# Kernel tuning notes

Hardware: AMD Instinct MI355X
Metric: run time of the kernel (lower is better)

The kernel has to match this reference:

```python
import math
import jax, jax.numpy as jnp
import numpy as np

N_EMBD = 1024
N_HEAD = 16
HEAD_DIM = N_EMBD // N_HEAD


def setup_inputs() -> dict:
    key = jax.random.key(0)
    ks = jax.random.split(key, 5)
    B, S = 4, 2048
    x = jax.random.normal(ks[0], (B, S, 2, N_EMBD), dtype=jnp.float32)
    Wt = jax.random.normal(ks[1], (N_EMBD, 3 * N_EMBD), dtype=jnp.float32) * 0.02
    Ws = jax.random.normal(ks[2], (N_EMBD, 2 * N_EMBD), dtype=jnp.float32) * 0.02
    Wo = jax.random.normal(ks[3], (N_EMBD, N_EMBD), dtype=jnp.float32) * 0.02
    lam_ts = jnp.ones((1,), dtype=jnp.float32)
    lam_st = jnp.ones((1,), dtype=jnp.float32)
    lam_ss = jnp.ones((1,), dtype=jnp.float32)
    return {"x": x, "Wt": Wt, "Ws": Ws, "Wo": Wo,
            "lam_ts": lam_ts, "lam_st": lam_st, "lam_ss": lam_ss}


def _heads(t, B, S):
    # [B,S,E] -> [B,H,S,D]
    return t.reshape(B, S, N_HEAD, HEAD_DIM).transpose(0, 2, 1, 3)


def reference(x, Wt, Ws, Wo, lam_ts, lam_st, lam_ss):
    B, S, _, E = x.shape
    xt = x[:, :, 0, :]  # text stream [B,S,E]
    xs = x[:, :, 1, :]  # spatial stream [B,S,E]

    qt, kt, vt = jnp.split(xt @ Wt, 3, axis=-1)
    qs, ks = jnp.split(xs @ Ws, 2, axis=-1)
    qt, kt, vt = _heads(qt, B, S), _heads(kt, B, S), _heads(vt, B, S)
    qs, ks = _heads(qs, B, S), _heads(ks, B, S)

    scale = 1.0 / math.sqrt(HEAD_DIM)
    att = (jnp.einsum('bhqd,bhkd->bhqk', qt, kt)
           + lam_ts[0] * jnp.einsum('bhqd,bhkd->bhqk', qt, ks)
           + lam_st[0] * jnp.einsum('bhqd,bhkd->bhqk', qs, kt)
           + lam_ss[0] * jnp.einsum('bhqd,bhkd->bhqk', qs, ks)) * scale
    att = jax.nn.softmax(att, axis=-1)

    y = jnp.einsum('bhqk,bhkd->bhqd', att, vt)  # [B,H,S,D]
    y = y.transpose(0, 2, 1, 3).reshape(B, S, E)
    y = y @ Wo
    # concat text output with untouched spatial stream -> [B,S,2,E]
    return jnp.concatenate([y[:, :, None, :], xs[:, :, None, :]], axis=2)
```

## Files before the change

### kernel.cpp

```cpp
#include <hip/hip_runtime.h>

typedef short  short8  __attribute__((ext_vector_type(8)));
typedef float  f32x4   __attribute__((ext_vector_type(4)));
typedef ushort u16x4   __attribute__((ext_vector_type(4)));

__device__ __forceinline__ float bf2f(ushort u) {
  union { unsigned u; float f; } v; v.u = ((unsigned)u) << 16; return v.f;
}
__device__ __forceinline__ ushort f2bf(float f) {
  union { float f; unsigned u; } v; v.f = f;
  unsigned r = v.u + 0x7FFF + ((v.u >> 16) & 1);
  return (ushort)(r >> 16);
}
__device__ __forceinline__ float exp2_fast(float x) {
  float r; asm("v_exp_f32 %0, %1" : "=v"(r) : "v"(x)); return r;
}

__device__ __forceinline__ void gload16(const ushort* g, ushort* l) {
  __builtin_amdgcn_global_load_lds(
      (__attribute__((address_space(1))) void*)(void*)(const_cast<ushort*>(g)),
      (__attribute__((address_space(3))) void*)(void*)l, 16, 0, 0);
}


__global__ __launch_bounds__(256) void prep_x(const float* __restrict__ x,
                                              ushort* __restrict__ xt,
                                              ushort* __restrict__ xs,
                                              float* __restrict__ out) {
  size_t i = ((size_t)blockIdx.x * 256 + threadIdx.x) * 4;
  size_t m = i >> 10, e = i & 1023;
  f32x4 a = *(const f32x4*)&x[m * 2048 + e];
  f32x4 b = *(const f32x4*)&x[m * 2048 + 1024 + e];
  u16x4 ta, tb;
#pragma unroll
  for (int j = 0; j < 4; ++j) { ta[j] = f2bf(a[j]); tb[j] = f2bf(b[j]); }
  *(u16x4*)&xt[i] = ta;
  *(u16x4*)&xs[i] = tb;
  *(f32x4*)&out[m * 2048 + 1024 + e] = b;
}

__global__ __launch_bounds__(256) void transpose_w(const float* __restrict__ W,
                                                   ushort* __restrict__ Wt,
                                                   int K, int N, int nq,
                                                   float qscale) {
  __shared__ float tile[32][33];
  int n0 = blockIdx.x * 32, k0 = blockIdx.y * 32;
  int tx = threadIdx.x & 31, ty = threadIdx.x >> 5;
#pragma unroll
  for (int i = 0; i < 32; i += 8)
    tile[ty + i][tx] = W[(size_t)(k0 + ty + i) * N + n0 + tx];
  __syncthreads();
#pragma unroll
  for (int i = 0; i < 32; i += 8) {
    int n = n0 + ty + i;
    float v = tile[tx][ty + i];
    if (n < nq) v *= qscale;
    Wt[(size_t)n * K + k0 + tx] = f2bf(v);
  }
}

template <int EPI>
__global__ __launch_bounds__(256) void gemm_bt(const ushort* __restrict__ A,
                                               const ushort* __restrict__ Bt,
                                               int N,
                                               ushort* __restrict__ o1,
                                               ushort* __restrict__ o2,
                                               const ushort* __restrict__ ct2,
                                               float* __restrict__ of,
                                               const float* plts,
                                               const float* plst,
                                               const float* plss) {
  const int K = 1024;
  __shared__ ushort sA[128 * 32];
  __shared__ ushort sB[128 * 32];
  const int tid = threadIdx.x;
  const int wave = tid >> 6, lane = tid & 63;
  const int wr = wave >> 1, wc = wave & 1;
  const int l15 = lane & 15, l4 = lane >> 4;
  const int m0 = blockIdx.y * 128, n0 = blockIdx.x * 128;

  f32x4 acc[4][4];
  const f32x4 z = {0.f, 0.f, 0.f, 0.f};
#pragma unroll
  for (int a = 0; a < 4; ++a)
#pragma unroll
    for (int b = 0; b < 4; ++b) acc[a][b] = z;

  for (int k0 = 0; k0 < K; k0 += 32) {
#pragma unroll
    for (int j = 0; j < 2; ++j) {
      int cb = j * 256 + wave * 64;
      int c = cb + lane;
      int row = c >> 2, cc = c & 3;
      gload16(&A [(size_t)(m0 + row) * K + k0 + cc * 8], &sA[cb * 8]);
      gload16(&Bt[(size_t)(n0 + row) * K + k0 + cc * 8], &sB[cb * 8]);
    }
    __syncthreads();
    short8 af[4], bfr[4];
#pragma unroll
    for (int i = 0; i < 4; ++i) {
      af[i]  = *(const short8*)&sA[(wr * 64 + i * 16 + l15) * 32 + l4 * 8];
      bfr[i] = *(const short8*)&sB[(wc * 64 + i * 16 + l15) * 32 + l4 * 8];
    }
#pragma unroll
    for (int mi = 0; mi < 4; ++mi)
#pragma unroll
      for (int ni = 0; ni < 4; ++ni)
        acc[mi][ni] = __builtin_amdgcn_mfma_f32_16x16x32_bf16(af[mi], bfr[ni], acc[mi][ni], 0, 0, 0);
    __syncthreads();
  }

  float lts = 0.f, lst = 0.f, lss = 0.f;
  if constexpr (EPI == 2) { lts = plts[0]; lst = plst[0]; lss = plss[0]; }

#pragma unroll
  for (int mi = 0; mi < 4; ++mi)
#pragma unroll
    for (int ni = 0; ni < 4; ++ni) {
      int rowb = m0 + wr * 64 + mi * 16 + l4 * 4;
      int col  = n0 + wc * 64 + ni * 16 + l15;
      if constexpr (EPI == 0) {
#pragma unroll
        for (int r = 0; r < 4; ++r)
          of[(size_t)(rowb + r) * 2048 + col] = acc[mi][ni][r];
      } else if constexpr (EPI == 1) {
        if (col < 1024) {
          int h = col >> 6, d = col & 63;
#pragma unroll
          for (int r = 0; r < 4; ++r) {
            int s = rowb + r, b = s >> 11, ss = s & 2047;
            o1[((size_t)(b * 16 + h) * 2048 + ss) * 128 + d] = f2bf(acc[mi][ni][r]);
          }
        } else {
#pragma unroll
          for (int r = 0; r < 4; ++r)
            o2[(size_t)(rowb + r) * 2048 + (col - 1024)] = f2bf(acc[mi][ni][r]);
        }
      } else {
        if (col < 1024) {
          int h = col >> 6, d = col & 63;
#pragma unroll
          for (int r = 0; r < 4; ++r) {
            int s = rowb + r, b = s >> 11, ss = s & 2047;
            o1[((size_t)(b * 16 + h) * 2048 + ss) * 128 + 64 + d] = f2bf(acc[mi][ni][r]);
          }
        } else {
          int d64 = col - 1024, h = d64 >> 6, d = d64 & 63;
#pragma unroll
          for (int r = 0; r < 4; ++r) {
            int s = rowb + r, b = s >> 11, ss = s & 2047;
            float kt = bf2f(ct2[(size_t)s * 2048 + d64]);
            float ks = acc[mi][ni][r];
            float k1 = kt + lts * ks;
            float k2 = lst * kt + lss * ks;
            size_t base = ((size_t)(b * 16 + h) * 2048 + ss) * 128;
            int off = ((((d >> 3) ^ (ss & 7)) << 3)) + (d & 7);
            o2[base + off]      = f2bf(k1);
            o2[base + 64 + off] = f2bf(k2);
          }
        }
      }
    }
}

__global__ __launch_bounds__(256) void transpose_v(const ushort* __restrict__ Ct2,
                                                   ushort* __restrict__ Vt) {
  int bh = blockIdx.y; int s0 = blockIdx.x * 64;
  int b = bh >> 4, h = bh & 15;
  __shared__ ushort t[64][72];
  int tid = threadIdx.x;
#pragma unroll
  for (int j = 0; j < 2; ++j) {
    int c = j * 256 + tid;
    int srow = c >> 3, cc = c & 7;
    *(short8*)&t[srow][cc * 8] =
        *(const short8*)&Ct2[(size_t)(b * 2048 + s0 + srow) * 2048 + 1024 + h * 64 + cc * 8];
  }
  __syncthreads();
#pragma unroll
  for (int j = 0; j < 2; ++j) {
    int c = j * 256 + tid;
    int drow = c >> 3, cc = c & 7;
    short8 v;
#pragma unroll
    for (int k = 0; k < 8; ++k) v[k] = t[cc * 8 + k][drow];
    *(short8*)&Vt[((size_t)bh * 64 + drow) * 2048 + s0 + ((cc ^ (drow & 7)) * 8)] = v;
  }
}

__global__ __launch_bounds__(256) void attn_kernel(const ushort* __restrict__ Q,
                                                   const ushort* __restrict__ Kg,
                                                   const ushort* __restrict__ Vg,
                                                   ushort* __restrict__ Y) {
  const int id   = blockIdx.x;
  const int virt = (id & 7) * 128 + (id >> 3);
  const int bh = virt >> 4;
  const int q0 = (virt & 15) * 128;
  const int tid = threadIdx.x;
  const int wave = tid >> 6, lane = tid & 63;
  const int l15 = lane & 15, l4 = lane >> 4;
  const size_t qkb = (size_t)bh * 2048 * 128;
  const size_t vb  = (size_t)bh * 64 * 2048;

  __shared__ ushort sKV[2 * 64 * 128 + 64 * 64];
  ushort* const sK0 = sKV;
  ushort* const sV  = sKV + 2 * 64 * 128;

  auto stageK = [&](int kv0, int bufi) {
    ushort* dK = sK0 + bufi * (64 * 128);
#pragma unroll
    for (int j = 0; j < 4; ++j) {
      int base = j * 256 + wave * 64;
      int c = base + lane, row = c >> 4, cc = c & 15;
      gload16(&Kg[qkb + (size_t)(kv0 + row) * 128 + cc * 8], &dK[base * 8]);
    }
  };
  auto stageV = [&](int kv0) {
#pragma unroll
    for (int j = 0; j < 2; ++j) {
      int base = j * 256 + wave * 64;
      int c = base + lane, row = c >> 3, cc = c & 7;
      gload16(&Vg[vb + (size_t)row * 2048 + kv0 + cc * 8], &sV[base * 8]);
    }
  };

  short8 qf[2][4];
#pragma unroll
  for (int qi = 0; qi < 2; ++qi) {
    int qrow = q0 + wave * 32 + qi * 16 + l15;
#pragma unroll
    for (int kk = 0; kk < 4; ++kk)
      qf[qi][kk] = *(const short8*)&Q[qkb + (size_t)qrow * 128 + kk * 32 + l4 * 8];
  }
  const f32x4 z = {0.f, 0.f, 0.f, 0.f};
  f32x4 accO[2][4] = {{z, z, z, z}, {z, z, z, z}};
  float mrow[2] = {-3.0e38f, -3.0e38f}, lrow[2] = {0.f, 0.f};

  stageK(0, 0);
  stageV(0);
  __syncthreads();

  for (int t = 0; t < 32; ++t) {
    const int cur = t & 1;
    if (t < 31) stageK((t + 1) * 64, cur ^ 1);
    const ushort* cK = sK0 + cur * (64 * 128);

    f32x4 sc[2][4] = {{z, z, z, z}, {z, z, z, z}};
    __builtin_amdgcn_s_setprio(1);
#pragma unroll
    for (int kk = 0; kk < 4; ++kk)
#pragma unroll
      for (int kb = 0; kb < 4; ++kb) {
        int row = kb * 16 + l15;
        const short8 kf = *(const short8*)&cK[row * 128 + (((kk * 4 + l4) ^ (row & 7)) * 8)];
        sc[0][kb] = __builtin_amdgcn_mfma_f32_16x16x32_bf16(kf, qf[0][kk], sc[0][kb], 0, 0, 0);
        sc[1][kb] = __builtin_amdgcn_mfma_f32_16x16x32_bf16(kf, qf[1][kk], sc[1][kb], 0, 0, 0);
      }
    __builtin_amdgcn_s_setprio(0);

    union { uint u4[4]; short8 s8; } pa[2][2];
#pragma unroll
    for (int qi = 0; qi < 2; ++qi) {
      float mx = sc[qi][0][0];
#pragma unroll
      for (int kb = 0; kb < 4; ++kb)
#pragma unroll
        for (int r = 0; r < 4; ++r) mx = fmaxf(mx, sc[qi][kb][r]);
      mx = fmaxf(mx, __shfl_xor(mx, 16));
      mx = fmaxf(mx, __shfl_xor(mx, 32));

      if (__any(mx > mrow[qi] + 8.f)) {
        float mnew = fmaxf(mrow[qi], mx);
        float corr = exp2_fast(mrow[qi] - mnew);
        mrow[qi] = mnew;
        lrow[qi] *= corr;
#pragma unroll
        for (int r = 0; r < 4; ++r) {
          float cq = __shfl(corr, l4 * 4 + r);
#pragma unroll
          for (int nf = 0; nf < 4; ++nf) accO[qi][nf][r] *= cq;
        }
      }

      float ps = 0.f;
#pragma unroll
      for (int kb = 0; kb < 4; ++kb)
#pragma unroll
        for (int r = 0; r < 4; ++r) {
          float e = exp2_fast(sc[qi][kb][r] - mrow[qi]);
          sc[qi][kb][r] = e; ps += e;
        }
      lrow[qi] += ps;

      uint u00, u01, u10, u11, u20, u21, u30, u31;
#define CVTPK(d, a, b) asm("v_cvt_pk_bf16_f32 %0, %1, %2" : "=v"(d) : "v"(a), "v"(b))
      CVTPK(u00, sc[qi][0][0], sc[qi][0][1]); CVTPK(u01, sc[qi][0][2], sc[qi][0][3]);
      CVTPK(u10, sc[qi][1][0], sc[qi][1][1]); CVTPK(u11, sc[qi][1][2], sc[qi][1][3]);
      CVTPK(u20, sc[qi][2][0], sc[qi][2][1]); CVTPK(u21, sc[qi][2][2], sc[qi][2][3]);
      CVTPK(u30, sc[qi][3][0], sc[qi][3][1]); CVTPK(u31, sc[qi][3][2], sc[qi][3][3]);
#undef CVTPK
      asm volatile("v_permlane32_swap_b32 %0, %1" : "+v"(u00), "+v"(u10));
      asm volatile("v_permlane32_swap_b32 %0, %1" : "+v"(u01), "+v"(u11));
      asm volatile("v_permlane32_swap_b32 %0, %1" : "+v"(u20), "+v"(u30));
      asm volatile("v_permlane32_swap_b32 %0, %1" : "+v"(u21), "+v"(u31));
      asm volatile("v_permlane16_swap_b32 %0, %1" : "+v"(u00), "+v"(u10));
      asm volatile("v_permlane16_swap_b32 %0, %1" : "+v"(u01), "+v"(u11));
      asm volatile("v_permlane16_swap_b32 %0, %1" : "+v"(u20), "+v"(u30));
      asm volatile("v_permlane16_swap_b32 %0, %1" : "+v"(u21), "+v"(u31));
      pa[qi][0].u4[0] = u00; pa[qi][0].u4[1] = u01; pa[qi][0].u4[2] = u10; pa[qi][0].u4[3] = u11;
      pa[qi][1].u4[0] = u20; pa[qi][1].u4[1] = u21; pa[qi][1].u4[2] = u30; pa[qi][1].u4[3] = u31;
    }

    __syncthreads();

    __builtin_amdgcn_s_setprio(1);
#pragma unroll
    for (int nf = 0; nf < 4; ++nf) {
      int d = nf * 16 + l15;
      const short8 vf0 = *(const short8*)&sV[d * 64 + ((l4 ^ (d & 7)) * 8)];
      const short8 vf1 = *(const short8*)&sV[d * 64 + (((4 + l4) ^ (d & 7)) * 8)];
      accO[0][nf] = __builtin_amdgcn_mfma_f32_16x16x32_bf16(pa[0][0].s8, vf0, accO[0][nf], 0, 0, 0);
      accO[1][nf] = __builtin_amdgcn_mfma_f32_16x16x32_bf16(pa[1][0].s8, vf0, accO[1][nf], 0, 0, 0);
      accO[0][nf] = __builtin_amdgcn_mfma_f32_16x16x32_bf16(pa[0][1].s8, vf1, accO[0][nf], 0, 0, 0);
      accO[1][nf] = __builtin_amdgcn_mfma_f32_16x16x32_bf16(pa[1][1].s8, vf1, accO[1][nf], 0, 0, 0);
    }
    __builtin_amdgcn_s_setprio(0);

    __syncthreads();
    if (t < 31) stageV((t + 1) * 64);
  }

  int b = bh >> 4, hh = bh & 15;
#pragma unroll
  for (int qi = 0; qi < 2; ++qi) {
    float ls = lrow[qi] + __shfl_xor(lrow[qi], 16);
    ls += __shfl_xor(ls, 32);
    float linv = 1.f / ls;
#pragma unroll
    for (int r = 0; r < 4; ++r) {
      float lq = __shfl(linv, l4 * 4 + r);
      int q = q0 + wave * 32 + qi * 16 + l4 * 4 + r;
#pragma unroll
      for (int nf = 0; nf < 4; ++nf)
        Y[((size_t)b * 2048 + q) * 1024 + hh * 64 + nf * 16 + l15] =
            f2bf(accO[qi][nf][r] * lq);
    }
  }
}

extern "C" void kernel_launch(void* const* d_in, const int* in_sizes, int n_in,
                              void* d_out, int out_size, void* d_ws, size_t ws_size,
                              hipStream_t stream) {
  const float* x   = (const float*)d_in[0];
  const float* Wt  = (const float*)d_in[1];
  const float* Ws  = (const float*)d_in[2];
  const float* Wo  = (const float*)d_in[3];
  const float* lts = (const float*)d_in[4];
  const float* lst = (const float*)d_in[5];
  const float* lss = (const float*)d_in[6];
  float* out = (float*)d_out;
  char* ws = (char*)d_ws;

  ushort* xt    = (ushort*)(ws + 0);
  ushort* xs    = (ushort*)(ws + 16777216);
  ushort* Wt_bt = (ushort*)(ws + 33554432);
  ushort* Ws_bt = (ushort*)(ws + 39845888);
  ushort* Wo_bt = (ushort*)(ws + 44040192);
  ushort* Ct2   = (ushort*)(ws + 46137344);
  ushort* Qbuf  = (ushort*)(ws + 79691776);
  ushort* Kbuf  = (ushort*)(ws + 113246208);
  ushort* Vtbuf = (ushort*)(ws + 146800640);
  ushort* Ybuf  = (ushort*)(ws + 163577856);
  (void)in_sizes; (void)n_in; (void)out_size; (void)ws_size;

  const float qscale = 0.125f * 1.44269504f;

  prep_x<<<8192, 256, 0, stream>>>(x, xt, xs, out);
  transpose_w<<<dim3(96, 32), 256, 0, stream>>>(Wt, Wt_bt, 1024, 3072, 1024, qscale);
  transpose_w<<<dim3(64, 32), 256, 0, stream>>>(Ws, Ws_bt, 1024, 2048, 1024, qscale);
  transpose_w<<<dim3(32, 32), 256, 0, stream>>>(Wo, Wo_bt, 1024, 1024, 0, 1.f);
  gemm_bt<1><<<dim3(24, 64), 256, 0, stream>>>(xt, Wt_bt, 3072, Qbuf, Ct2,
                                               nullptr, nullptr, nullptr, nullptr, nullptr);
  gemm_bt<2><<<dim3(16, 64), 256, 0, stream>>>(xs, Ws_bt, 2048, Qbuf, Kbuf,
                                               Ct2, nullptr, lts, lst, lss);
  transpose_v<<<dim3(32, 64), 256, 0, stream>>>(Ct2, Vtbuf);
  attn_kernel<<<1024, 256, 0, stream>>>(Qbuf, Kbuf, Vtbuf, Ybuf);
  gemm_bt<0><<<dim3(8, 64), 256, 0, stream>>>(Ybuf, Wo_bt, 1024, nullptr, nullptr,
                                              nullptr, out, nullptr, nullptr, nullptr);
}
```

Measured before the change: 323.8 us.

## Replace QKV projection GEMMs with 256x256 double-buffered pipelined kernel

The two input-projection GEMMs now use a new 512-thread kernel with 256x256 output tiles and K-step 64. LDS is double-buffered and XOR-swizzled, global-to-LDS loads for the next K tile are interleaved between MFMA phases, and block IDs are remapped across XCDs. The aim is more data reuse per tile and overlap of memory latency with compute. In exchange it uses 128KB of LDS and many accumulator registers, and the grids are small (384 and 256 blocks), so occupancy and tail effects are a risk. The output projection keeps the old 128x128 kernel, split out as a non-templated version.

```diff
diff --git a/kernel.cpp b/kernel.cpp
--- a/kernel.cpp
+++ b/kernel.cpp
@@ -59,17 +59,9 @@
   }
 }
 
-template <int EPI>
-__global__ __launch_bounds__(256) void gemm_bt(const ushort* __restrict__ A,
-                                               const ushort* __restrict__ Bt,
-                                               int N,
-                                               ushort* __restrict__ o1,
-                                               ushort* __restrict__ o2,
-                                               const ushort* __restrict__ ct2,
-                                               float* __restrict__ of,
-                                               const float* plts,
-                                               const float* plst,
-                                               const float* plss) {
+__global__ __launch_bounds__(256) void gemm_bt0(const ushort* __restrict__ A,
+                                                const ushort* __restrict__ Bt,
+                                                float* __restrict__ of) {
   const int K = 1024;
   __shared__ ushort sA[128 * 32];
   __shared__ ushort sB[128 * 32];
@@ -110,31 +102,134 @@
     __syncthreads();
   }
 
+#pragma unroll
+  for (int mi = 0; mi < 4; ++mi)
+#pragma unroll
+    for (int ni = 0; ni < 4; ++ni) {
+      int row = m0 + wr * 64 + mi * 16 + l4 * 4;
+      int col = n0 + wc * 64 + ni * 16 + l15;
+#pragma unroll
+      for (int r = 0; r < 4; ++r)
+        of[(size_t)(row + r) * 2048 + col] = acc[mi][ni][r];
+    }
+}
+
+template <int EPI>
+__global__ __launch_bounds__(512, 2) void gemm256(const ushort* __restrict__ A,
+                                                  const ushort* __restrict__ Bt,
+                                                  int NTN,
+                                                  ushort* __restrict__ o1,
+                                                  ushort* __restrict__ o2,
+                                                  const ushort* __restrict__ ct2,
+                                                  const float* plts,
+                                                  const float* plst,
+                                                  const float* plss) {
+  __shared__ ushort lds[65536];
+  const int tid = threadIdx.x;
+  const int wave = tid >> 6, lane = tid & 63;
+  const int wr = wave >> 2, wc = wave & 3;
+  const int l15 = lane & 15, l4 = lane >> 4;
+
+  const int cpx = gridDim.x >> 3;
+  const int v = (blockIdx.x & 7) * cpx + (blockIdx.x >> 3);
+  const int m0 = (v / NTN) * 256, n0 = (v % NTN) * 256;
+
+  const int swz2 = (l15 >> 2) & 3;
+  const int kp0 = (l4 * 8) ^ (swz2 << 4);
+  const int kp1 = (32 + l4 * 8) ^ (swz2 << 4);
+
+  auto stage_half = [&](int kt0, int half, int buf) {
+    const ushort* src = (half < 2) ? A : Bt;
+    int rbase = (half < 2) ? (m0 + (half << 7)) : (n0 + ((half - 2) << 7));
+    int lbase = ((half < 2) ? 0 : 32768) + buf * 16384 + (half & 1) * 8192;
+#pragma unroll
+    for (int j = 0; j < 2; ++j) {
+      int c = j * 512 + tid;
+      int m = c >> 3, kc = c & 7;
+      int kcs = kc ^ (((m >> 2) & 3) << 1);
+      gload16(&src[(size_t)(rbase + m) * 1024 + kt0 + kcs * 8], &lds[lbase + c * 8]);
+    }
+  };
+
+  f32x4 acc[8][4];
+  const f32x4 z = {0.f, 0.f, 0.f, 0.f};
+#pragma unroll
+  for (int a = 0; a < 8; ++a)
+#pragma unroll
+    for (int b = 0; b < 4; ++b) acc[a][b] = z;
+
+  const int aBase = wr * 8192 + l15 * 64;
+  const int bBase = 32768 + (wc >> 1) * 8192 + ((wc & 1) * 64 + l15) * 64;
+
+  stage_half(0, 0, 0); stage_half(0, 1, 0); stage_half(0, 2, 0); stage_half(0, 3, 0);
+
+  for (int t = 0; t < 16; ++t) {
+    const int abuf = (t & 1) * 16384;
+    const int nbuf = 1 - (t & 1);
+    const int kt1 = (t + 1) * 64;
+    short8 bfr[4][2];
+
+    if (t < 15) stage_half(kt1, 0, nbuf);
+    if (t < 15) asm volatile("s_waitcnt vmcnt(2)" ::: "memory");
+    else        asm volatile("s_waitcnt vmcnt(0)" ::: "memory");
+    __builtin_amdgcn_s_barrier();
+    __builtin_amdgcn_sched_barrier(0);
+#pragma unroll
+    for (int nf = 0; nf < 4; ++nf) {
+      bfr[nf][0] = *(const short8*)&lds[abuf + bBase + nf * 1024 + kp0];
+      bfr[nf][1] = *(const short8*)&lds[abuf + bBase + nf * 1024 + kp1];
+    }
+#define GPH_MFMA(MF0)                                                          \
+    {                                                                          \
+      short8 a00 = *(const short8*)&lds[abuf + aBase + (MF0) * 1024 + kp0];    \
+      short8 a01 = *(const short8*)&lds[abuf + aBase + (MF0) * 1024 + kp1];    \
+      short8 a10 = *(const short8*)&lds[abuf + aBase + (MF0 + 1) * 1024 + kp0];\
+      short8 a11 = *(const short8*)&lds[abuf + aBase + (MF0 + 1) * 1024 + kp1];\
+      __builtin_amdgcn_s_setprio(1);                                           \
+      _Pragma("unroll")                                                        \
+      for (int nf = 0; nf < 4; ++nf) {                                         \
+        acc[MF0][nf]     = __builtin_amdgcn_mfma_f32_16x16x32_bf16(a00, bfr[nf][0], acc[MF0][nf], 0, 0, 0);     \
+        acc[MF0][nf]     = __builtin_amdgcn_mfma_f32_16x16x32_bf16(a01, bfr[nf][1], acc[MF0][nf], 0, 0, 0);     \
+        acc[MF0 + 1][nf] = __builtin_amdgcn_mfma_f32_16x16x32_bf16(a10, bfr[nf][0], acc[MF0 + 1][nf], 0, 0, 0); \
+        acc[MF0 + 1][nf] = __builtin_amdgcn_mfma_f32_16x16x32_bf16(a11, bfr[nf][1], acc[MF0 + 1][nf], 0, 0, 0); \
+      }                                                                        \
+      __builtin_amdgcn_s_setprio(0);                                           \
+    }                                                                          \
+    __builtin_amdgcn_s_barrier();                                              \
+    __builtin_amdgcn_sched_barrier(0);
+
+    GPH_MFMA(0)
+    if (t < 15) stage_half(kt1, 1, nbuf);
+    GPH_MFMA(2)
+    if (t < 15) stage_half(kt1, 2, nbuf);
+    GPH_MFMA(4)
+    if (t < 15) stage_half(kt1, 3, nbuf);
+    GPH_MFMA(6)
+#undef GPH_MFMA
+  }
+
   float lts = 0.f, lst = 0.f, lss = 0.f;
   if constexpr (EPI == 2) { lts = plts[0]; lst = plst[0]; lss = plss[0]; }
-
-#pragma unroll
-  for (int mi = 0; mi < 4; ++mi)
-#pragma unroll
-    for (int ni = 0; ni < 4; ++ni) {
-      int rowb = m0 + wr * 64 + mi * 16 + l4 * 4;
-      int col  = n0 + wc * 64 + ni * 16 + l15;
-      if constexpr (EPI == 0) {
-#pragma unroll
-        for (int r = 0; r < 4; ++r)
-          of[(size_t)(rowb + r) * 2048 + col] = acc[mi][ni][r];
-      } else if constexpr (EPI == 1) {
+  (void)ct2;
+
+#pragma unroll
+  for (int mf = 0; mf < 8; ++mf)
+#pragma unroll
+    for (int nf = 0; nf < 4; ++nf) {
+      int rowb = m0 + wr * 128 + mf * 16 + l4 * 4;
+      int col  = n0 + wc * 64 + nf * 16 + l15;
+      if constexpr (EPI == 1) {
         if (col < 1024) {
           int h = col >> 6, d = col & 63;
 #pragma unroll
           for (int r = 0; r < 4; ++r) {
             int s = rowb + r, b = s >> 11, ss = s & 2047;
-            o1[((size_t)(b * 16 + h) * 2048 + ss) * 128 + d] = f2bf(acc[mi][ni][r]);
+            o1[((size_t)(b * 16 + h) * 2048 + ss) * 128 + d] = f2bf(acc[mf][nf][r]);
           }
         } else {
 #pragma unroll
           for (int r = 0; r < 4; ++r)
-            o2[(size_t)(rowb + r) * 2048 + (col - 1024)] = f2bf(acc[mi][ni][r]);
+            o2[(size_t)(rowb + r) * 2048 + (col - 1024)] = f2bf(acc[mf][nf][r]);
         }
       } else {
         if (col < 1024) {
@@ -142,7 +237,7 @@
 #pragma unroll
           for (int r = 0; r < 4; ++r) {
             int s = rowb + r, b = s >> 11, ss = s & 2047;
-            o1[((size_t)(b * 16 + h) * 2048 + ss) * 128 + 64 + d] = f2bf(acc[mi][ni][r]);
+            o1[((size_t)(b * 16 + h) * 2048 + ss) * 128 + 64 + d] = f2bf(acc[mf][nf][r]);
           }
         } else {
           int d64 = col - 1024, h = d64 >> 6, d = d64 & 63;
@@ -150,7 +245,7 @@
           for (int r = 0; r < 4; ++r) {
             int s = rowb + r, b = s >> 11, ss = s & 2047;
             float kt = bf2f(ct2[(size_t)s * 2048 + d64]);
-            float ks = acc[mi][ni][r];
+            float ks = acc[mf][nf][r];
             float k1 = kt + lts * ks;
             float k2 = lst * kt + lss * ks;
             size_t base = ((size_t)(b * 16 + h) * 2048 + ss) * 128;
@@ -379,12 +474,11 @@
   transpose_w<<<dim3(96, 32), 256, 0, stream>>>(Wt, Wt_bt, 1024, 3072, 1024, qscale);
   transpose_w<<<dim3(64, 32), 256, 0, stream>>>(Ws, Ws_bt, 1024, 2048, 1024, qscale);
   transpose_w<<<dim3(32, 32), 256, 0, stream>>>(Wo, Wo_bt, 1024, 1024, 0, 1.f);
-  gemm_bt<1><<<dim3(24, 64), 256, 0, stream>>>(xt, Wt_bt, 3072, Qbuf, Ct2,
-                                               nullptr, nullptr, nullptr, nullptr, nullptr);
-  gemm_bt<2><<<dim3(16, 64), 256, 0, stream>>>(xs, Ws_bt, 2048, Qbuf, Kbuf,
-                                               Ct2, nullptr, lts, lst, lss);
+  gemm256<1><<<384, 512, 0, stream>>>(xt, Wt_bt, 12, Qbuf, Ct2,
+                                      nullptr, nullptr, nullptr, nullptr);
+  gemm256<2><<<256, 512, 0, stream>>>(xs, Ws_bt, 8, Qbuf, Kbuf,
+                                      Ct2, lts, lst, lss);
   transpose_v<<<dim3(32, 64), 256, 0, stream>>>(Ct2, Vtbuf);
   attn_kernel<<<1024, 256, 0, stream>>>(Qbuf, Kbuf, Vtbuf, Ybuf);
-  gemm_bt<0><<<dim3(8, 64), 256, 0, stream>>>(Ybuf, Wo_bt, 1024, nullptr, nullptr,
-                                              nullptr, out, nullptr, nullptr, nullptr);
-}
+  gemm_bt0<<<dim3(8, 64), 256, 0, stream>>>(Ybuf, Wo_bt, out);
+}
```

Result: faster. 314.9 us (-2.8%).
